# Kernel tuning notes

Measured on AMD Instinct MI355X. Metric: run time of the kernel, lower is better.

Reference implementation:

```python
import jax, jax.numpy as jnp
import numpy as np

N = 65536          # number of rows (nodes/edges)
F = 64             # input feature dim
UNITS = 64         # output dim
NUM_RELATIONS = 25
NUM_BASES = 8


def setup_inputs() -> dict:
    key = jax.random.key(0)
    k1, k2, k3, k4 = jax.random.split(key, 4)
    features = jax.random.normal(k1, (N, F), dtype=jnp.float32)
    relations = jax.random.randint(k2, (N,), 0, NUM_RELATIONS, dtype=jnp.int32)
    # basis kernels V_b: [B, F, units] (glorot-like scale)
    kernel = jax.random.normal(k3, (NUM_BASES, F, UNITS), dtype=jnp.float32) * (1.0 / np.sqrt(F))
    # basis coefficients a_rb: [R, B]
    lin_bases = jax.random.normal(k4, (NUM_RELATIONS, NUM_BASES), dtype=jnp.float32) * (1.0 / np.sqrt(NUM_BASES))
    bias = jnp.zeros((UNITS,), dtype=jnp.float32)
    return {"features": features, "relations": relations, "kernel": kernel,
            "lin_bases": lin_bases, "bias": bias}


def reference(features, relations, kernel, lin_bases, bias):
    # Basis decomposition: W_r = sum_b a_rb V_b  -> [R, F, units]
    w = jnp.einsum('rb,bfo->rfo', lin_bases, kernel)
    # Gather per-row kernel and contract (matches ops.take + batch_dot)
    w_per_row = w[relations]                       # [N, F, units]
    out = jnp.einsum('nf,nfo->no', features, w_per_row)  # [N, units]
    out = out + bias
    return out  # linear activation (activation=None)
```

## Files before the change

kernel.cpp:

```cpp
#include <hip/hip_runtime.h>


typedef float v4f __attribute__((ext_vector_type(4)));
typedef short bf16x8 __attribute__((ext_vector_type(8)));
typedef float f32x4 __attribute__((ext_vector_type(4)));
typedef unsigned short u16;
typedef u16 u16x4 __attribute__((ext_vector_type(4)));

#define NN 65536
#define FF 64
#define UU 64
#define RR 25
#define BB 8
#define SBN 64
#define CAPB 96
#define NSLOT (RR * SBN * CAPB)
#define SAS 72

#define IDX_OFF  0
#define BCNT_OFF (NSLOT * 4)
#define WT_OFF   (BCNT_OFF + SBN * RR * 4)
#define WS_NEED  ((size_t)(WT_OFF + RR * FF * UU * 2))

__device__ __forceinline__ u16 f2bf(float x) {
  union { float f; unsigned u; } v; v.f = x;
  unsigned r = v.u + 0x7FFF + ((v.u >> 16) & 1);
  return (u16)(r >> 16);
}

__global__ __launch_bounds__(256) void k_prep(
    const float* __restrict__ kern,
    const float* __restrict__ lin,
    const int*   __restrict__ rel,
    u16*         __restrict__ Wt,
    int*         __restrict__ idx_sorted,
    int*         __restrict__ bcnt) {
  const int wblocks = (RR * FF * UU) / 256;
  int bid = blockIdx.x;
  if (bid < wblocks) {
    int idx = bid * 256 + threadIdx.x;
    int r = __builtin_amdgcn_readfirstlane(idx >> 12);
    int f = (idx >> 6) & 63;
    int u = idx & 63;
    float acc = 0.f;
#pragma unroll
    for (int b = 0; b < BB; ++b)
      acc += lin[r * BB + b] * kern[b * (FF * UU) + f * UU + u];
    Wt[r * (FF * UU) + u * FF + f] = f2bf(acc);
  } else {
    int sb  = bid - wblocks;
    int tid = threadIdx.x;
    __shared__ int cnt[RR];
    if (tid < RR) cnt[tid] = 0;
    __syncthreads();
#pragma unroll
    for (int j = 0; j < 4; ++j) {
      int row  = sb * 1024 + j * 256 + tid;
      int r    = rel[row];
      int rank = atomicAdd(&cnt[r], 1);
      if (rank < CAPB)
        idx_sorted[(r * SBN + sb) * CAPB + rank] = row;
    }
    __syncthreads();
    if (tid < RR) bcnt[sb * RR + tid] = cnt[tid];
  }
}

__global__ __launch_bounds__(256, 4) void k_main(
    const float* __restrict__ features,
    const float* __restrict__ bias,
    const u16*   __restrict__ Wt,
    const int*   __restrict__ idx_sorted,
    const int*   __restrict__ bcnt,
    float*       __restrict__ out) {
  __shared__ u16 sA[CAPB * SAS];

  int tid = threadIdx.x;
  int b   = blockIdx.x;
  int r   = __builtin_amdgcn_readfirstlane(b >> 6);
  int sb  = b & 63;
  int valid = bcnt[sb * RR + r];
  if (valid <= 0) return;
  if (valid > CAPB) valid = CAPB;

  int base = (r * SBN + sb) * CAPB;

  int lane = tid & 63;
  int w    = __builtin_amdgcn_readfirstlane(tid >> 6);
  int m    = lane & 15;
  int quad = lane >> 4;

  const bf16x8* wrow = reinterpret_cast<const bf16x8*>(Wt + (size_t)r * (FF * UU));
  bf16x8 bfrag[2];
#pragma unroll
  for (int h = 0; h < 2; ++h)
    bfrag[h] = wrow[(w * 16 + m) * 8 + h * 4 + quad];
  float bv = bias[w * 16 + m];

  const v4f* f4 = reinterpret_cast<const v4f*>(features);
#pragma unroll
  for (int i = 0; i < 6; ++i) {
    int s   = i * 256 + tid;
    int rl  = s >> 4;
    int seg = s & 15;
    if (rl < valid) {
      int grow = idx_sorted[base + rl];
      v4f fv = f4[(size_t)grow * 16 + seg];
      u16x4 p = { f2bf(fv[0]), f2bf(fv[1]), f2bf(fv[2]), f2bf(fv[3]) };
      *reinterpret_cast<u16x4*>(&sA[rl * SAS + seg * 4]) = p;
    }
  }
  __syncthreads();

  int nt = (valid + 15) >> 4;

  for (int t = 0; t < nt; ++t) {
    f32x4 acc = (f32x4){bv, bv, bv, bv};
#pragma unroll
    for (int h = 0; h < 2; ++h) {
      bf16x8 afrag = *reinterpret_cast<const bf16x8*>(
          &sA[(t * 16 + m) * SAS + h * 32 + quad * 8]);
      acc = __builtin_amdgcn_mfma_f32_16x16x32_bf16(afrag, bfrag[h], acc, 0, 0, 0);
    }
#pragma unroll
    for (int g = 0; g < 4; ++g) {
      int orow = t * 16 + quad * 4 + g;
      if (orow < valid) {
        int grow = idx_sorted[base + orow];
        out[(size_t)grow * UU + w * 16 + m] = acc[g];
      }
    }
  }
}

__global__ __launch_bounds__(256) void k_fallback(
    const float* __restrict__ features,
    const int*   __restrict__ rel,
    const float* __restrict__ kern,
    const float* __restrict__ lin,
    const float* __restrict__ bias,
    float*       __restrict__ out) {
  int tid = threadIdx.x;
  int row = blockIdx.x * 64 + (tid & 63);
  int q   = __builtin_amdgcn_readfirstlane(tid >> 6);
  int r   = rel[row];
  float cf[BB];
#pragma unroll
  for (int b = 0; b < BB; ++b) cf[b] = lin[r * BB + b];
  const v4f* fr = reinterpret_cast<const v4f*>(features + (size_t)row * FF);
  float acc[16];
#pragma unroll
  for (int j = 0; j < 16; ++j) acc[j] = bias[q * 16 + j];
#pragma unroll
  for (int ch = 0; ch < 4; ++ch) {
    v4f fv[4];
#pragma unroll
    for (int k = 0; k < 4; ++k) fv[k] = fr[ch * 4 + k];
#pragma unroll
    for (int k = 0; k < 4; ++k) {
#pragma unroll
      for (int c = 0; c < 4; ++c) {
        int f = ch * 16 + k * 4 + c;
        float fs = fv[k][c];
        float wf[16];
#pragma unroll
        for (int jj = 0; jj < 16; ++jj) wf[jj] = 0.f;
#pragma unroll
        for (int b = 0; b < BB; ++b) {
          const float* Vb = kern + b * (FF * UU) + f * UU + q * 16;
#pragma unroll
          for (int jj = 0; jj < 16; ++jj) wf[jj] += cf[b] * Vb[jj];
        }
#pragma unroll
        for (int jj = 0; jj < 16; ++jj) acc[jj] += fs * wf[jj];
      }
    }
  }
  v4f* o4 = reinterpret_cast<v4f*>(out + (size_t)row * UU + q * 16);
#pragma unroll
  for (int j4 = 0; j4 < 4; ++j4) {
    v4f v = {acc[4 * j4], acc[4 * j4 + 1], acc[4 * j4 + 2], acc[4 * j4 + 3]};
    o4[j4] = v;
  }
}

extern "C" void kernel_launch(void* const* d_in, const int* in_sizes, int n_in,
                              void* d_out, int out_size, void* d_ws, size_t ws_size,
                              hipStream_t stream) {
  const float* features  = (const float*)d_in[0];
  const int*   relations = (const int*)d_in[1];
  const float* kern      = (const float*)d_in[2];
  const float* lin       = (const float*)d_in[3];
  const float* bias      = (const float*)d_in[4];
  float* out = (float*)d_out;

  if (ws_size >= WS_NEED) {
    char* ws         = (char*)d_ws;
    int*  idx_sorted = (int*)(ws + IDX_OFF);
    int*  bcnt       = (int*)(ws + BCNT_OFF);
    u16*  Wt         = (u16*)(ws + WT_OFF);
    k_prep<<<(RR * FF * UU) / 256 + SBN, 256, 0, stream>>>(
        kern, lin, relations, Wt, idx_sorted, bcnt);
    k_main<<<RR * SBN, 256, 0, stream>>>(features, bias, Wt, idx_sorted, bcnt, out);
  } else {
    k_fallback<<<NN / 64, 256, 0, stream>>>(features, relations, kern, lin, bias, out);
  }
}
```

Baseline: 82.43 us.

## Replace relation bucketing with single fused kernel projecting onto all bases

Removes the prep kernel that built per-relation weights and bucketed rows by relation. A single kernel now processes contiguous 128-row tiles, multiplies each row by all 8 basis kernels with MFMA, and combines the results with per-row basis coefficients loaded from lin_bases. This drops the extra launch, the scattered gathers and the index indirection, and it also removes the CAPB bucket-overflow limit. In exchange it does 8x the MFMA work and each block converts the basis kernel to bf16 with strided global loads.

After: 81.55 us. About the same (-1.1%).

```diff
diff --git a/kernel.cpp b/kernel.cpp
--- a/kernel.cpp
+++ b/kernel.cpp
@@ -12,15 +12,8 @@
 #define UU 64
 #define RR 25
 #define BB 8
-#define SBN 64
-#define CAPB 96
-#define NSLOT (RR * SBN * CAPB)
+#define ROWS 128
 #define SAS 72
-
-#define IDX_OFF  0
-#define BCNT_OFF (NSLOT * 4)
-#define WT_OFF   (BCNT_OFF + SBN * RR * 4)
-#define WS_NEED  ((size_t)(WT_OFF + RR * FF * UU * 2))
 
 __device__ __forceinline__ u16 f2bf(float x) {
   union { float f; unsigned u; } v; v.f = x;
@@ -28,159 +21,81 @@
   return (u16)(r >> 16);
 }
 
-__global__ __launch_bounds__(256) void k_prep(
-    const float* __restrict__ kern,
-    const float* __restrict__ lin,
-    const int*   __restrict__ rel,
-    u16*         __restrict__ Wt,
-    int*         __restrict__ idx_sorted,
-    int*         __restrict__ bcnt) {
-  const int wblocks = (RR * FF * UU) / 256;
-  int bid = blockIdx.x;
-  if (bid < wblocks) {
-    int idx = bid * 256 + threadIdx.x;
-    int r = __builtin_amdgcn_readfirstlane(idx >> 12);
-    int f = (idx >> 6) & 63;
-    int u = idx & 63;
-    float acc = 0.f;
-#pragma unroll
-    for (int b = 0; b < BB; ++b)
-      acc += lin[r * BB + b] * kern[b * (FF * UU) + f * UU + u];
-    Wt[r * (FF * UU) + u * FF + f] = f2bf(acc);
-  } else {
-    int sb  = bid - wblocks;
-    int tid = threadIdx.x;
-    __shared__ int cnt[RR];
-    if (tid < RR) cnt[tid] = 0;
-    __syncthreads();
-#pragma unroll
-    for (int j = 0; j < 4; ++j) {
-      int row  = sb * 1024 + j * 256 + tid;
-      int r    = rel[row];
-      int rank = atomicAdd(&cnt[r], 1);
-      if (rank < CAPB)
-        idx_sorted[(r * SBN + sb) * CAPB + rank] = row;
-    }
-    __syncthreads();
-    if (tid < RR) bcnt[sb * RR + tid] = cnt[tid];
-  }
-}
-
-__global__ __launch_bounds__(256, 4) void k_main(
-    const float* __restrict__ features,
-    const float* __restrict__ bias,
-    const u16*   __restrict__ Wt,
-    const int*   __restrict__ idx_sorted,
-    const int*   __restrict__ bcnt,
-    float*       __restrict__ out) {
-  __shared__ u16 sA[CAPB * SAS];
-
-  int tid = threadIdx.x;
-  int b   = blockIdx.x;
-  int r   = __builtin_amdgcn_readfirstlane(b >> 6);
-  int sb  = b & 63;
-  int valid = bcnt[sb * RR + r];
-  if (valid <= 0) return;
-  if (valid > CAPB) valid = CAPB;
-
-  int base = (r * SBN + sb) * CAPB;
-
-  int lane = tid & 63;
-  int w    = __builtin_amdgcn_readfirstlane(tid >> 6);
-  int m    = lane & 15;
-  int quad = lane >> 4;
-
-  const bf16x8* wrow = reinterpret_cast<const bf16x8*>(Wt + (size_t)r * (FF * UU));
-  bf16x8 bfrag[2];
-#pragma unroll
-  for (int h = 0; h < 2; ++h)
-    bfrag[h] = wrow[(w * 16 + m) * 8 + h * 4 + quad];
-  float bv = bias[w * 16 + m];
-
-  const v4f* f4 = reinterpret_cast<const v4f*>(features);
-#pragma unroll
-  for (int i = 0; i < 6; ++i) {
-    int s   = i * 256 + tid;
-    int rl  = s >> 4;
-    int seg = s & 15;
-    if (rl < valid) {
-      int grow = idx_sorted[base + rl];
-      v4f fv = f4[(size_t)grow * 16 + seg];
-      u16x4 p = { f2bf(fv[0]), f2bf(fv[1]), f2bf(fv[2]), f2bf(fv[3]) };
-      *reinterpret_cast<u16x4*>(&sA[rl * SAS + seg * 4]) = p;
-    }
-  }
-  __syncthreads();
-
-  int nt = (valid + 15) >> 4;
-
-  for (int t = 0; t < nt; ++t) {
-    f32x4 acc = (f32x4){bv, bv, bv, bv};
-#pragma unroll
-    for (int h = 0; h < 2; ++h) {
-      bf16x8 afrag = *reinterpret_cast<const bf16x8*>(
-          &sA[(t * 16 + m) * SAS + h * 32 + quad * 8]);
-      acc = __builtin_amdgcn_mfma_f32_16x16x32_bf16(afrag, bfrag[h], acc, 0, 0, 0);
-    }
-#pragma unroll
-    for (int g = 0; g < 4; ++g) {
-      int orow = t * 16 + quad * 4 + g;
-      if (orow < valid) {
-        int grow = idx_sorted[base + orow];
-        out[(size_t)grow * UU + w * 16 + m] = acc[g];
-      }
-    }
-  }
-}
-
-__global__ __launch_bounds__(256) void k_fallback(
+__global__ __launch_bounds__(256, 3) void k_fused(
     const float* __restrict__ features,
     const int*   __restrict__ rel,
     const float* __restrict__ kern,
     const float* __restrict__ lin,
     const float* __restrict__ bias,
     float*       __restrict__ out) {
-  int tid = threadIdx.x;
-  int row = blockIdx.x * 64 + (tid & 63);
-  int q   = __builtin_amdgcn_readfirstlane(tid >> 6);
-  int r   = rel[row];
-  float cf[BB];
+  __shared__ u16   sA[ROWS * SAS];
+  __shared__ float scoef[ROWS][BB];
+
+  int tid  = threadIdx.x;
+  int row0 = blockIdx.x * ROWS;
+
+  {
+    int rl = tid >> 1, half = tid & 1;
+    int r  = rel[row0 + rl];
+    const v4f* lv = reinterpret_cast<const v4f*>(lin);
+    *reinterpret_cast<v4f*>(&scoef[rl][half * 4]) = lv[r * 2 + half];
+  }
+
+  const v4f* f4 = reinterpret_cast<const v4f*>(features);
 #pragma unroll
-  for (int b = 0; b < BB; ++b) cf[b] = lin[r * BB + b];
-  const v4f* fr = reinterpret_cast<const v4f*>(features + (size_t)row * FF);
-  float acc[16];
+  for (int i = 0; i < (ROWS * 16) / 256; ++i) {
+    int s   = i * 256 + tid;
+    int rl  = s >> 4;
+    int seg = s & 15;
+    v4f fv = f4[(size_t)(row0 + rl) * 16 + seg];
+    u16x4 p = { f2bf(fv[0]), f2bf(fv[1]), f2bf(fv[2]), f2bf(fv[3]) };
+    *reinterpret_cast<u16x4*>(&sA[rl * SAS + seg * 4]) = p;
+  }
+
+  int lane = tid & 63;
+  int w    = __builtin_amdgcn_readfirstlane(tid >> 6);
+  int m    = lane & 15;
+  int quad = lane >> 4;
+  int col  = w * 16 + m;
+
+  bf16x8 bfrag[BB][2];
 #pragma unroll
-  for (int j = 0; j < 16; ++j) acc[j] = bias[q * 16 + j];
+  for (int b = 0; b < BB; ++b) {
 #pragma unroll
-  for (int ch = 0; ch < 4; ++ch) {
-    v4f fv[4];
+    for (int h = 0; h < 2; ++h) {
+      const float* vp = kern + b * (FF * UU) + (h * 32 + quad * 8) * UU + col;
+      bf16x8 v;
 #pragma unroll
-    for (int k = 0; k < 4; ++k) fv[k] = fr[ch * 4 + k];
-#pragma unroll
-    for (int k = 0; k < 4; ++k) {
-#pragma unroll
-      for (int c = 0; c < 4; ++c) {
-        int f = ch * 16 + k * 4 + c;
-        float fs = fv[k][c];
-        float wf[16];
-#pragma unroll
-        for (int jj = 0; jj < 16; ++jj) wf[jj] = 0.f;
-#pragma unroll
-        for (int b = 0; b < BB; ++b) {
-          const float* Vb = kern + b * (FF * UU) + f * UU + q * 16;
-#pragma unroll
-          for (int jj = 0; jj < 16; ++jj) wf[jj] += cf[b] * Vb[jj];
-        }
-#pragma unroll
-        for (int jj = 0; jj < 16; ++jj) acc[jj] += fs * wf[jj];
-      }
+      for (int j = 0; j < 8; ++j)
+        v[j] = (short)f2bf(vp[j * UU]);
+      bfrag[b][h] = v;
     }
   }
-  v4f* o4 = reinterpret_cast<v4f*>(out + (size_t)row * UU + q * 16);
+
+  float bv = bias[col];
+  __syncthreads();
+
+  const f32x4 zero = (f32x4){0.f, 0.f, 0.f, 0.f};
 #pragma unroll
-  for (int j4 = 0; j4 < 4; ++j4) {
-    v4f v = {acc[4 * j4], acc[4 * j4 + 1], acc[4 * j4 + 2], acc[4 * j4 + 3]};
-    o4[j4] = v;
+  for (int t = 0; t < ROWS / 16; ++t) {
+    bf16x8 af0 = *reinterpret_cast<const bf16x8*>(&sA[(t * 16 + m) * SAS + quad * 8]);
+    bf16x8 af1 = *reinterpret_cast<const bf16x8*>(&sA[(t * 16 + m) * SAS + 32 + quad * 8]);
+    f32x4 acc[BB];
+#pragma unroll
+    for (int b = 0; b < BB; ++b) {
+      acc[b] = __builtin_amdgcn_mfma_f32_16x16x32_bf16(af0, bfrag[b][0], zero, 0, 0, 0);
+      acc[b] = __builtin_amdgcn_mfma_f32_16x16x32_bf16(af1, bfrag[b][1], acc[b], 0, 0, 0);
+    }
+#pragma unroll
+    for (int g = 0; g < 4; ++g) {
+      int rl = t * 16 + quad * 4 + g;
+      v4f c0 = *reinterpret_cast<const v4f*>(&scoef[rl][0]);
+      v4f c1 = *reinterpret_cast<const v4f*>(&scoef[rl][4]);
+      float o = bv;
+      o += c0[0] * acc[0][g] + c0[1] * acc[1][g] + c0[2] * acc[2][g] + c0[3] * acc[3][g];
+      o += c1[0] * acc[4][g] + c1[1] * acc[5][g] + c1[2] * acc[6][g] + c1[3] * acc[7][g];
+      out[(size_t)(row0 + rl) * UU + col] = o;
+    }
   }
 }
 
@@ -193,16 +108,7 @@
   const float* lin       = (const float*)d_in[3];
   const float* bias      = (const float*)d_in[4];
   float* out = (float*)d_out;
+  (void)d_ws; (void)ws_size;
 
-  if (ws_size >= WS_NEED) {
-    char* ws         = (char*)d_ws;
-    int*  idx_sorted = (int*)(ws + IDX_OFF);
-    int*  bcnt       = (int*)(ws + BCNT_OFF);
-    u16*  Wt         = (u16*)(ws + WT_OFF);
-    k_prep<<<(RR * FF * UU) / 256 + SBN, 256, 0, stream>>>(
-        kern, lin, relations, Wt, idx_sorted, bcnt);
-    k_main<<<RR * SBN, 256, 0, stream>>>(features, bias, Wt, idx_sorted, bcnt, out);
-  } else {
-    k_fallback<<<NN / 64, 256, 0, stream>>>(features, relations, kern, lin, bias, out);
-  }
+  k_fused<<<NN / ROWS, 256, 0, stream>>>(features, relations, kern, lin, bias, out);
 }
```
